# Kernel tuning notes

Measured on AMD Instinct MI355X. Metric: run time of the kernel, lower is better.

The kernel has to match this reference:

```python
import jax, jax.numpy as jnp
import numpy as np

D_MODEL = 1024
N_HEADS = 16
HEAD_DIM = D_MODEL // N_HEADS  # 64
THETA = 10000.0
BATCH = 2
SEQ = 2048


def _init_weight(k):
    std = np.sqrt(2.0 / (D_MODEL + D_MODEL)).astype(np.float32)
    return jax.random.truncated_normal(k, -3.0, 3.0, (D_MODEL, D_MODEL), jnp.float32) * std


def setup_inputs() -> dict:
    key = jax.random.key(0)
    kx, kq, kk, kv, ko = jax.random.split(key, 5)
    x = jax.random.normal(kx, (BATCH, SEQ, D_MODEL), jnp.float32)
    token_positions = jnp.arange(SEQ, dtype=jnp.int32)
    return {
        "x": x,
        "token_positions": token_positions,
        "Wq": _init_weight(kq),
        "Wk": _init_weight(kk),
        "Wv": _init_weight(kv),
        "Wo": _init_weight(ko),
    }


def _rope(x, token_positions):
    # x: (B, H, S, HEAD_DIM), token_positions: (S,)
    pair_idx = jnp.arange(0, HEAD_DIM, 2, dtype=jnp.float32)
    inv_freq = 1.0 / (THETA ** (pair_idx / HEAD_DIM))        # (HEAD_DIM/2,)
    angles = token_positions.astype(jnp.float32)[:, None] * inv_freq  # (S, HEAD_DIM/2)
    cos = jnp.cos(angles).astype(x.dtype)
    sin = jnp.sin(angles).astype(x.dtype)
    x_even = x[..., 0::2]
    x_odd = x[..., 1::2]
    out_even = x_even * cos - x_odd * sin
    out_odd = x_even * sin + x_odd * cos
    return jnp.stack((out_even, out_odd), axis=-1).reshape(x.shape)


def reference(x, token_positions, Wq, Wk, Wv, Wo):
    B, S, _ = x.shape

    def proj(W):  # (B,S,D) @ (D,D)^T -> (B,H,S,HEAD_DIM)
        return (x @ W.T).reshape(B, S, N_HEADS, HEAD_DIM).transpose(0, 2, 1, 3)

    q = _rope(proj(Wq), token_positions)
    k = _rope(proj(Wk), token_positions)
    v = proj(Wv)

    scale = 1.0 / np.sqrt(HEAD_DIM).astype(np.float32)
    scores = jnp.einsum('bhqd,bhkd->bhqk', q, k) * scale  # (B,H,S,S)
    causal = jnp.tril(jnp.ones((S, S), dtype=bool))
    scores = jnp.where(causal, scores, -jnp.inf)
    probs = jax.nn.softmax(scores.astype(jnp.float32), axis=-1).astype(x.dtype)

    attn = jnp.einsum('bhqk,bhkd->bhqd', probs, v)  # (B,H,S,HEAD_DIM)
    attn = attn.transpose(0, 2, 1, 3).reshape(B, S, D_MODEL)
    return attn @ Wo.T
```

## Files before the change

kernel.cpp:

```cpp
#include <hip/hip_runtime.h>

typedef __bf16 bf16x4 __attribute__((ext_vector_type(4)));
typedef __bf16 bf16x8 __attribute__((ext_vector_type(8)));
typedef float floatx4 __attribute__((ext_vector_type(4)));

#define MFMA16(a, b, c) __builtin_amdgcn_mfma_f32_16x16x32_bf16((a), (b), (c), 0, 0, 0)

#define GLD16(gptr, lptr)                                                      \
    __builtin_amdgcn_global_load_lds(                                          \
        (const __attribute__((address_space(1))) void*)(gptr),                 \
        (__attribute__((address_space(3))) void*)(lptr), 16, 0, 0)

constexpr int D_MODEL = 1024;
constexpr int SEQ = 2048;
constexpr int HEAD_DIM = 64;
constexpr int M_TOK = 2 * SEQ;
constexpr int N_HEADS = 16;
constexpr float ROPE_C = 0.20762050593048596f;

__global__ __launch_bounds__(256) void convert_all(
    const float* __restrict__ x,  const float* __restrict__ wq,
    const float* __restrict__ wk, const float* __restrict__ wv,
    const float* __restrict__ wo, __bf16* __restrict__ dst,
    const int* __restrict__ pos, float2* __restrict__ rt)
{
    const size_t i = ((size_t)blockIdx.x * 256 + threadIdx.x) * 8;
    const float* s;
    size_t off;
    if (i < 4194304) { s = x; off = i; }
    else {
        const int w = (int)((i - 4194304) >> 20);
        off = (i - 4194304) & 1048575;
        s = (w == 0) ? wq : (w == 1) ? wk : (w == 2) ? wv : wo;
    }
    const floatx4 lo = *(const floatx4*)(s + off);
    const floatx4 hi = *(const floatx4*)(s + off + 4);
    bf16x8 v;
    v[0] = (__bf16)lo[0]; v[1] = (__bf16)lo[1]; v[2] = (__bf16)lo[2]; v[3] = (__bf16)lo[3];
    v[4] = (__bf16)hi[0]; v[5] = (__bf16)hi[1]; v[6] = (__bf16)hi[2]; v[7] = (__bf16)hi[3];
    *(bf16x8*)(dst + i) = v;

    const int gid = blockIdx.x * 256 + threadIdx.x;
    if (gid < SEQ * 32) {
        const int p = gid >> 5, j = gid & 31;
        const float ang = (float)pos[p] * exp2f(-(float)(2 * j) * ROPE_C);
        rt[gid] = make_float2(cosf(ang), sinf(ang));
    }
}

template<int MODE>
__global__ __launch_bounds__(256, 2) void gemm_tiled(
    const __bf16* __restrict__ A, const __bf16* __restrict__ B,
    __bf16* __restrict__ Qb, __bf16* __restrict__ Kb, __bf16* __restrict__ Vt,
    float* __restrict__ Cf, const float2* __restrict__ rt)
{
    __shared__ __bf16 As[128 * 32];
    __shared__ __bf16 Bs[128 * 32];
    const int tid  = threadIdx.x;
    const int wave = tid >> 6, lane = tid & 63;
    const int quad = lane >> 4, l16 = lane & 15;
    const int m0 = blockIdx.x * 128, n0 = blockIdx.y * 128;
    const int wm = (wave >> 1) * 64, wn = (wave & 1) * 64;

    floatx4 c00 = {}, c01 = {}, c02 = {}, c03 = {};
    floatx4 c10 = {}, c11 = {}, c12 = {}, c13 = {};
    floatx4 c20 = {}, c21 = {}, c22 = {}, c23 = {};
    floatx4 c30 = {}, c31 = {}, c32 = {}, c33 = {};

    const int sm = tid >> 2;
    const int sk = (tid & 3) * 8;
    const __bf16* gA = A + (size_t)(m0 + sm) * D_MODEL + sk;
    const __bf16* gB = B + (size_t)(n0 + sm) * D_MODEL + sk;
    __bf16* lAs0 = &As[wave * 512];
    __bf16* lAs1 = &As[2048 + wave * 512];
    __bf16* lBs0 = &Bs[wave * 512];
    __bf16* lBs1 = &Bs[2048 + wave * 512];

    for (int k0 = 0; k0 < D_MODEL; k0 += 32) {
        __syncthreads();
        GLD16(gA + k0,                          lAs0);
        GLD16(gA + (size_t)64 * D_MODEL + k0,   lAs1);
        GLD16(gB + k0,                          lBs0);
        GLD16(gB + (size_t)64 * D_MODEL + k0,   lBs1);
        __syncthreads();

        const bf16x8 a0 = *(const bf16x8*)&As[(wm      + l16) * 32 + quad * 8];
        const bf16x8 a1 = *(const bf16x8*)&As[(wm + 16 + l16) * 32 + quad * 8];
        const bf16x8 a2 = *(const bf16x8*)&As[(wm + 32 + l16) * 32 + quad * 8];
        const bf16x8 a3 = *(const bf16x8*)&As[(wm + 48 + l16) * 32 + quad * 8];
        const bf16x8 b0 = *(const bf16x8*)&Bs[(wn      + l16) * 32 + quad * 8];
        const bf16x8 b1 = *(const bf16x8*)&Bs[(wn + 16 + l16) * 32 + quad * 8];
        const bf16x8 b2 = *(const bf16x8*)&Bs[(wn + 32 + l16) * 32 + quad * 8];
        const bf16x8 b3 = *(const bf16x8*)&Bs[(wn + 48 + l16) * 32 + quad * 8];

        c00 = MFMA16(a0, b0, c00); c01 = MFMA16(a0, b1, c01);
        c02 = MFMA16(a0, b2, c02); c03 = MFMA16(a0, b3, c03);
        c10 = MFMA16(a1, b0, c10); c11 = MFMA16(a1, b1, c11);
        c12 = MFMA16(a1, b2, c12); c13 = MFMA16(a1, b3, c13);
        c20 = MFMA16(a2, b0, c20); c21 = MFMA16(a2, b1, c21);
        c22 = MFMA16(a2, b2, c22); c23 = MFMA16(a2, b3, c23);
        c30 = MFMA16(a3, b0, c30); c31 = MFMA16(a3, b1, c31);
        c32 = MFMA16(a3, b2, c32); c33 = MFMA16(a3, b3, c33);
    }

#define EPI(I, J, CV) do {                                                     \
        const int n  = n0 + wn + (J) * 16 + l16;                               \
        const int t0 = m0 + wm + (I) * 16 + quad * 4;                          \
        if (MODE == 1) {                                                       \
            Cf[(size_t)(t0 + 0) * D_MODEL + n] = (CV)[0];                      \
            Cf[(size_t)(t0 + 1) * D_MODEL + n] = (CV)[1];                      \
            Cf[(size_t)(t0 + 2) * D_MODEL + n] = (CV)[2];                      \
            Cf[(size_t)(t0 + 3) * D_MODEL + n] = (CV)[3];                      \
        } else {                                                               \
            const int region = n >> 10, col = n & 1023;                        \
            if (region == 2) {                                                 \
                bf16x4 v;                                                      \
                v[0] = (__bf16)(CV)[0]; v[1] = (__bf16)(CV)[1];                \
                v[2] = (__bf16)(CV)[2]; v[3] = (__bf16)(CV)[3];                \
                const size_t vidx =                                            \
                    ((size_t)(t0 >> 11) * 1024 + col) * SEQ + (t0 & (SEQ - 1));\
                *(bf16x4*)(Vt + vidx) = v;                                     \
            } else {                                                           \
                const int d = col & (HEAD_DIM - 1);                            \
                const int j = d >> 1;                                          \
                __bf16* dst = (region == 0) ? Qb : Kb;                         \
                _Pragma("unroll")                                              \
                for (int r = 0; r < 4; ++r) {                                  \
                    float v = (CV)[r];                                         \
                    const float vp = __shfl_xor(v, 1);                         \
                    const float2 cs =                                          \
                        rt[(size_t)((t0 + r) & (SEQ - 1)) * 32 + j];           \
                    v = (d & 1) ? (vp * cs.y + v * cs.x)                       \
                                : (v * cs.x - vp * cs.y);                      \
                    dst[(size_t)(t0 + r) * D_MODEL + col] = (__bf16)v;         \
                }                                                              \
            }                                                                  \
        }                                                                      \
    } while (0)

    EPI(0, 0, c00); EPI(0, 1, c01); EPI(0, 2, c02); EPI(0, 3, c03);
    EPI(1, 0, c10); EPI(1, 1, c11); EPI(1, 2, c12); EPI(1, 3, c13);
    EPI(2, 0, c20); EPI(2, 1, c21); EPI(2, 2, c22); EPI(2, 3, c23);
    EPI(3, 0, c30); EPI(3, 1, c31); EPI(3, 2, c32); EPI(3, 3, c33);
#undef EPI
}

__global__ __launch_bounds__(256, 4) void attn_fused(
    const __bf16* Q, const __bf16* __restrict__ K,
    const __bf16* __restrict__ Vt, __bf16* O)
{
    const int tid  = threadIdx.x;
    const int wave = tid >> 6, lane = tid & 63;
    const int quad = lane >> 4, l16 = lane & 15;

    const int wgid = blockIdx.x + 16 * blockIdx.y;
    const int xcd  = wgid & 7;
    const int slot = wgid >> 3;
    const int bh   = (xcd << 2) | (slot >> 4);
    const int bx   = slot & 15;

    const size_t base  = (size_t)(bh >> 4) * SEQ * D_MODEL + (size_t)(bh & 15) * HEAD_DIM;
    const __bf16* kbase  = K + base;
    const __bf16* vtbase = Vt + (size_t)bh * HEAD_DIM * SEQ;

    __shared__ __bf16 Ks[64][72];
    __shared__ __bf16 Vs[64][72];
    __shared__ __bf16 P[4][16][72];

    constexpr float C2 = 0.18033688011112042f;
    const int sr = tid >> 2;
    const int sc = (tid & 3) * 16;

    auto process_tile = [&](int T) {
        const int Q0  = T * 64;
        const int q0w = Q0 + wave * 16;
        const int qg  = q0w + l16;

        const __bf16* qrow = Q + base + (size_t)(q0w + l16) * D_MODEL + quad * 8;
        const bf16x8 qf0 = *(const bf16x8*)(qrow);
        const bf16x8 qf1 = *(const bf16x8*)(qrow + 32);

        float mm = -__builtin_inff(), l_i = 0.f;
        floatx4 o0 = {}, o1 = {}, o2 = {}, o3 = {};

        for (int k0 = 0; k0 <= Q0; k0 += 64) {
            __syncthreads();
            {
                const __bf16* kgp = kbase + (size_t)(k0 + sr) * D_MODEL + sc;
                *(bf16x8*)&Ks[sr][sc]     = *(const bf16x8*)(kgp);
                *(bf16x8*)&Ks[sr][sc + 8] = *(const bf16x8*)(kgp + 8);
                const __bf16* vgp = vtbase + (size_t)sr * SEQ + k0 + sc;
                *(bf16x8*)&Vs[sr][sc]     = *(const bf16x8*)(vgp);
                *(bf16x8*)&Vs[sr][sc + 8] = *(const bf16x8*)(vgp + 8);
            }
            __syncthreads();

            floatx4 s0 = {}, s1 = {}, s2 = {}, s3 = {};
            s0 = MFMA16(*(const bf16x8*)&Ks[l16][quad * 8],      qf0, s0);
            s0 = MFMA16(*(const bf16x8*)&Ks[l16][32 + quad * 8], qf1, s0);
            s1 = MFMA16(*(const bf16x8*)&Ks[16 + l16][quad * 8],      qf0, s1);
            s1 = MFMA16(*(const bf16x8*)&Ks[16 + l16][32 + quad * 8], qf1, s1);
            s2 = MFMA16(*(const bf16x8*)&Ks[32 + l16][quad * 8],      qf0, s2);
            s2 = MFMA16(*(const bf16x8*)&Ks[32 + l16][32 + quad * 8], qf1, s2);
            s3 = MFMA16(*(const bf16x8*)&Ks[48 + l16][quad * 8],      qf0, s3);
            s3 = MFMA16(*(const bf16x8*)&Ks[48 + l16][32 + quad * 8], qf1, s3);

            if (k0 == Q0) {
#pragma unroll
                for (int r = 0; r < 4; ++r) {
                    const int kb = k0 + quad * 4 + r;
                    if (kb      > qg) s0[r] = -__builtin_inff();
                    if (kb + 16 > qg) s1[r] = -__builtin_inff();
                    if (kb + 32 > qg) s2[r] = -__builtin_inff();
                    if (kb + 48 > qg) s3[r] = -__builtin_inff();
                }
            }

            float mx = fmaxf(fmaxf(fmaxf(s0[0], s0[1]), fmaxf(s0[2], s0[3])),
                             fmaxf(fmaxf(s1[0], s1[1]), fmaxf(s1[2], s1[3])));
            mx = fmaxf(mx, fmaxf(fmaxf(fmaxf(s2[0], s2[1]), fmaxf(s2[2], s2[3])),
                                 fmaxf(fmaxf(s3[0], s3[1]), fmaxf(s3[2], s3[3]))));
            mx = fmaxf(mx, __shfl_xor(mx, 16));
            mx = fmaxf(mx, __shfl_xor(mx, 32));
            const float mmn  = fmaxf(mm, mx * C2);
            const float alpha = exp2f(mm - mmn);
            float rs = 0.f;
#pragma unroll
            for (int r = 0; r < 4; ++r) {
                s0[r] = exp2f(s0[r] * C2 - mmn);
                s1[r] = exp2f(s1[r] * C2 - mmn);
                s2[r] = exp2f(s2[r] * C2 - mmn);
                s3[r] = exp2f(s3[r] * C2 - mmn);
                rs += s0[r] + s1[r] + s2[r] + s3[r];
            }
            rs += __shfl_xor(rs, 16);
            rs += __shfl_xor(rs, 32);
            l_i = l_i * alpha + rs;
            mm = mmn;
            o0 *= alpha; o1 *= alpha; o2 *= alpha; o3 *= alpha;

            bf16x4 pw0, pw1, pw2, pw3;
#pragma unroll
            for (int r = 0; r < 4; ++r) {
                pw0[r] = (__bf16)s0[r]; pw1[r] = (__bf16)s1[r];
                pw2[r] = (__bf16)s2[r]; pw3[r] = (__bf16)s3[r];
            }
            *(bf16x4*)&P[wave][l16][quad * 4]      = pw0;
            *(bf16x4*)&P[wave][l16][16 + quad * 4] = pw1;
            *(bf16x4*)&P[wave][l16][32 + quad * 4] = pw2;
            *(bf16x4*)&P[wave][l16][48 + quad * 4] = pw3;
            const bf16x8 pp0 = *(const bf16x8*)&P[wave][l16][quad * 8];
            const bf16x8 pp1 = *(const bf16x8*)&P[wave][l16][32 + quad * 8];

            o0 = MFMA16(*(const bf16x8*)&Vs[l16][quad * 8],      pp0, o0);
            o0 = MFMA16(*(const bf16x8*)&Vs[l16][32 + quad * 8], pp1, o0);
            o1 = MFMA16(*(const bf16x8*)&Vs[16 + l16][quad * 8],      pp0, o1);
            o1 = MFMA16(*(const bf16x8*)&Vs[16 + l16][32 + quad * 8], pp1, o1);
            o2 = MFMA16(*(const bf16x8*)&Vs[32 + l16][quad * 8],      pp0, o2);
            o2 = MFMA16(*(const bf16x8*)&Vs[32 + l16][32 + quad * 8], pp1, o2);
            o3 = MFMA16(*(const bf16x8*)&Vs[48 + l16][quad * 8],      pp0, o3);
            o3 = MFMA16(*(const bf16x8*)&Vs[48 + l16][32 + quad * 8], pp1, o3);
        }

        const float rl = 1.0f / l_i;
        __bf16* orow = O + base + (size_t)(q0w + l16) * D_MODEL + quad * 4;
        bf16x4 w0, w1, w2, w3;
#pragma unroll
        for (int r = 0; r < 4; ++r) {
            w0[r] = (__bf16)(o0[r] * rl);
            w1[r] = (__bf16)(o1[r] * rl);
            w2[r] = (__bf16)(o2[r] * rl);
            w3[r] = (__bf16)(o3[r] * rl);
        }
        *(bf16x4*)(orow)      = w0;
        *(bf16x4*)(orow + 16) = w1;
        *(bf16x4*)(orow + 32) = w2;
        *(bf16x4*)(orow + 48) = w3;
    };

    process_tile(bx);
    process_tile(31 - bx);
}

extern "C" void kernel_launch(void* const* d_in, const int* in_sizes, int n_in,
                              void* d_out, int out_size, void* d_ws, size_t ws_size,
                              hipStream_t stream) {
    const int* pos = (const int*)d_in[1];
    float* out = (float*)d_out;

    const size_t xe = (size_t)M_TOK * D_MODEL;
    const size_t we = (size_t)D_MODEL * D_MODEL;
    __bf16* Xb = (__bf16*)d_ws;
    __bf16* Wb = Xb + xe;
    __bf16* Qb = Wb + 4 * we;
    __bf16* Kb = Qb + xe;
    __bf16* Vt = Kb + xe;
    float2* rt = (float2*)d_out;

    convert_all<<<4096, 256, 0, stream>>>(
        (const float*)d_in[0], (const float*)d_in[2], (const float*)d_in[3],
        (const float*)d_in[4], (const float*)d_in[5], Xb, pos, rt);

    gemm_tiled<0><<<dim3(M_TOK / 128, 3072 / 128), 256, 0, stream>>>(
        Xb, Wb, Qb, Kb, Vt, nullptr, rt);

    attn_fused<<<dim3(16, 2 * N_HEADS), 256, 0, stream>>>(Qb, Kb, Vt, Qb);

    gemm_tiled<1><<<dim3(M_TOK / 128, D_MODEL / 128), 256, 0, stream>>>(
        Qb, Wb + 3 * we, nullptr, nullptr, nullptr, out, rt);
}
```

Baseline: 193.8 us.

## Double-buffer K/V tiles in attention with register prefetch

The attention kernel now keeps two LDS buffers for K and V. The next tile is loaded from global memory into registers at the top of each iteration and written to the alternate buffer after the softmax, so one of the two barriers per iteration goes away and global load latency overlaps with the QK MFMAs and the softmax. In exchange it doubles K/V shared memory, which may reduce occupancy, and adds register pressure. Correctness depends on a single barrier guarding reuse of the alternate buffer.

```diff
diff --git a/kernel.cpp b/kernel.cpp
--- a/kernel.cpp
+++ b/kernel.cpp
@@ -163,8 +163,8 @@
     const __bf16* kbase  = K + base;
     const __bf16* vtbase = Vt + (size_t)bh * HEAD_DIM * SEQ;
 
-    __shared__ __bf16 Ks[64][72];
-    __shared__ __bf16 Vs[64][72];
+    __shared__ __bf16 Ks[2][64][72];
+    __shared__ __bf16 Vs[2][64][72];
     __shared__ __bf16 P[4][16][72];
 
     constexpr float C2 = 0.18033688011112042f;
@@ -183,27 +183,43 @@
         float mm = -__builtin_inff(), l_i = 0.f;
         floatx4 o0 = {}, o1 = {}, o2 = {}, o3 = {};
 
+        bf16x8 kr0, kr1, vr0, vr1;
+        {
+            const __bf16* kgp = kbase + (size_t)sr * D_MODEL + sc;
+            kr0 = *(const bf16x8*)(kgp);
+            kr1 = *(const bf16x8*)(kgp + 8);
+            const __bf16* vgp = vtbase + (size_t)sr * SEQ + sc;
+            vr0 = *(const bf16x8*)(vgp);
+            vr1 = *(const bf16x8*)(vgp + 8);
+        }
+        __syncthreads();
+        *(bf16x8*)&Ks[0][sr][sc]     = kr0;
+        *(bf16x8*)&Ks[0][sr][sc + 8] = kr1;
+        *(bf16x8*)&Vs[0][sr][sc]     = vr0;
+        *(bf16x8*)&Vs[0][sr][sc + 8] = vr1;
+        int cur = 0;
+
         for (int k0 = 0; k0 <= Q0; k0 += 64) {
+            const bool pf = (k0 + 64 <= Q0);
+            if (pf) {
+                const __bf16* kgp = kbase + (size_t)(k0 + 64 + sr) * D_MODEL + sc;
+                kr0 = *(const bf16x8*)(kgp);
+                kr1 = *(const bf16x8*)(kgp + 8);
+                const __bf16* vgp = vtbase + (size_t)sr * SEQ + (k0 + 64) + sc;
+                vr0 = *(const bf16x8*)(vgp);
+                vr1 = *(const bf16x8*)(vgp + 8);
+            }
             __syncthreads();
-            {
-                const __bf16* kgp = kbase + (size_t)(k0 + sr) * D_MODEL + sc;
-                *(bf16x8*)&Ks[sr][sc]     = *(const bf16x8*)(kgp);
-                *(bf16x8*)&Ks[sr][sc + 8] = *(const bf16x8*)(kgp + 8);
-                const __bf16* vgp = vtbase + (size_t)sr * SEQ + k0 + sc;
-                *(bf16x8*)&Vs[sr][sc]     = *(const bf16x8*)(vgp);
-                *(bf16x8*)&Vs[sr][sc + 8] = *(const bf16x8*)(vgp + 8);
-            }
-            __syncthreads();
 
             floatx4 s0 = {}, s1 = {}, s2 = {}, s3 = {};
-            s0 = MFMA16(*(const bf16x8*)&Ks[l16][quad * 8],      qf0, s0);
-            s0 = MFMA16(*(const bf16x8*)&Ks[l16][32 + quad * 8], qf1, s0);
-            s1 = MFMA16(*(const bf16x8*)&Ks[16 + l16][quad * 8],      qf0, s1);
-            s1 = MFMA16(*(const bf16x8*)&Ks[16 + l16][32 + quad * 8], qf1, s1);
-            s2 = MFMA16(*(const bf16x8*)&Ks[32 + l16][quad * 8],      qf0, s2);
-            s2 = MFMA16(*(const bf16x8*)&Ks[32 + l16][32 + quad * 8], qf1, s2);
-            s3 = MFMA16(*(const bf16x8*)&Ks[48 + l16][quad * 8],      qf0, s3);
-            s3 = MFMA16(*(const bf16x8*)&Ks[48 + l16][32 + quad * 8], qf1, s3);
+            s0 = MFMA16(*(const bf16x8*)&Ks[cur][l16][quad * 8],      qf0, s0);
+            s0 = MFMA16(*(const bf16x8*)&Ks[cur][l16][32 + quad * 8], qf1, s0);
+            s1 = MFMA16(*(const bf16x8*)&Ks[cur][16 + l16][quad * 8],      qf0, s1);
+            s1 = MFMA16(*(const bf16x8*)&Ks[cur][16 + l16][32 + quad * 8], qf1, s1);
+            s2 = MFMA16(*(const bf16x8*)&Ks[cur][32 + l16][quad * 8],      qf0, s2);
+            s2 = MFMA16(*(const bf16x8*)&Ks[cur][32 + l16][32 + quad * 8], qf1, s2);
+            s3 = MFMA16(*(const bf16x8*)&Ks[cur][48 + l16][quad * 8],      qf0, s3);
+            s3 = MFMA16(*(const bf16x8*)&Ks[cur][48 + l16][32 + quad * 8], qf1, s3);
 
             if (k0 == Q0) {
 #pragma unroll
@@ -239,6 +255,13 @@
             mm = mmn;
             o0 *= alpha; o1 *= alpha; o2 *= alpha; o3 *= alpha;
 
+            if (pf) {
+                *(bf16x8*)&Ks[cur ^ 1][sr][sc]     = kr0;
+                *(bf16x8*)&Ks[cur ^ 1][sr][sc + 8] = kr1;
+                *(bf16x8*)&Vs[cur ^ 1][sr][sc]     = vr0;
+                *(bf16x8*)&Vs[cur ^ 1][sr][sc + 8] = vr1;
+            }
+
             bf16x4 pw0, pw1, pw2, pw3;
 #pragma unroll
             for (int r = 0; r < 4; ++r) {
@@ -252,14 +275,15 @@
             const bf16x8 pp0 = *(const bf16x8*)&P[wave][l16][quad * 8];
             const bf16x8 pp1 = *(const bf16x8*)&P[wave][l16][32 + quad * 8];
 
-            o0 = MFMA16(*(const bf16x8*)&Vs[l16][quad * 8],      pp0, o0);
-            o0 = MFMA16(*(const bf16x8*)&Vs[l16][32 + quad * 8], pp1, o0);
-            o1 = MFMA16(*(const bf16x8*)&Vs[16 + l16][quad * 8],      pp0, o1);
-            o1 = MFMA16(*(const bf16x8*)&Vs[16 + l16][32 + quad * 8], pp1, o1);
-            o2 = MFMA16(*(const bf16x8*)&Vs[32 + l16][quad * 8],      pp0, o2);
-            o2 = MFMA16(*(const bf16x8*)&Vs[32 + l16][32 + quad * 8], pp1, o2);
-            o3 = MFMA16(*(const bf16x8*)&Vs[48 + l16][quad * 8],      pp0, o3);
-            o3 = MFMA16(*(const bf16x8*)&Vs[48 + l16][32 + quad * 8], pp1, o3);
+            o0 = MFMA16(*(const bf16x8*)&Vs[cur][l16][quad * 8],      pp0, o0);
+            o0 = MFMA16(*(const bf16x8*)&Vs[cur][l16][32 + quad * 8], pp1, o0);
+            o1 = MFMA16(*(const bf16x8*)&Vs[cur][16 + l16][quad * 8],      pp0, o1);
+            o1 = MFMA16(*(const bf16x8*)&Vs[cur][16 + l16][32 + quad * 8], pp1, o1);
+            o2 = MFMA16(*(const bf16x8*)&Vs[cur][32 + l16][quad * 8],      pp0, o2);
+            o2 = MFMA16(*(const bf16x8*)&Vs[cur][32 + l16][32 + quad * 8], pp1, o2);
+            o3 = MFMA16(*(const bf16x8*)&Vs[cur][48 + l16][quad * 8],      pp0, o3);
+            o3 = MFMA16(*(const bf16x8*)&Vs[cur][48 + l16][32 + quad * 8], pp1, o3);
+            cur ^= 1;
         }
 
         const float rl = 1.0f / l_i;
```

Result: no change. 193.8 us (+0.0%).
